# Optimization experiments

Hardware: AMD Instinct MI355X
Metric: run time of the kernel (lower is better)

Reference implementation:

```python
import jax, jax.numpy as jnp
import numpy as np

EPS = 1e-6

def _ln(x):
    # LayerNorm without affine, biased variance (matches torch default)
    m = jnp.mean(x, axis=-1, keepdims=True)
    v = jnp.var(x, axis=-1, keepdims=True)
    return (x - m) / jnp.sqrt(v + EPS)

def setup_inputs() -> dict:
    key = jax.random.key(0)
    ks = jax.random.split(key, 12)
    B, N, C = 8, 4096, 768
    H = C * 4
    s = 0.02
    return {
        "x":   jax.random.normal(ks[0], (B, N, C), dtype=jnp.float32),
        "Wq":  jax.random.normal(ks[1], (C, C), dtype=jnp.float32) * s,
        "bq":  jnp.zeros((C,), dtype=jnp.float32),
        "Wkv": jax.random.normal(ks[2], (C, 2 * C), dtype=jnp.float32) * s,
        "bkv": jnp.zeros((2 * C,), dtype=jnp.float32),
        "Wo":  jax.random.normal(ks[3], (C, C), dtype=jnp.float32) * s,
        "bo":  jnp.zeros((C,), dtype=jnp.float32),
        "W1":  jax.random.normal(ks[4], (C, H), dtype=jnp.float32) * s,
        "b1":  jnp.zeros((H,), dtype=jnp.float32),
        "W2":  jax.random.normal(ks[5], (H, C), dtype=jnp.float32) * s,
        "b2":  jnp.zeros((C,), dtype=jnp.float32),
    }

def reference(x, Wq, bq, Wkv, bkv, Wo, bo, W1, b1, W2, b2):
    B, N, C = x.shape
    h = 16
    d = C // h
    scale = d ** -0.5

    xn = _ln(x)                          # norm1 over full sequence
    past = xn[:, :-1, :]                 # [B, N-1, C]
    cur = xn[:, -1, :]                   # [B, C]

    q = (cur @ Wq + bq).reshape(B, h, 1, d)                 # [B,h,1,d]
    kv = past @ Wkv + bkv                                   # [B,N-1,2C]
    k, v = jnp.split(kv, 2, axis=-1)
    k = k.reshape(B, N - 1, h, d).transpose(0, 2, 1, 3)     # [B,h,N-1,d]
    v = v.reshape(B, N - 1, h, d).transpose(0, 2, 1, 3)

    sim = jnp.einsum('bhqd,bhkd->bhqk', q, k) * scale       # [B,h,1,N-1]
    attn = jax.nn.softmax(sim, axis=-1)
    out = jnp.einsum('bhqk,bhkd->bhqd', attn, v)            # [B,h,1,d]
    out = out.transpose(0, 2, 1, 3).reshape(B, C)           # [B,C]
    out = out @ Wo + bo

    last = x[:, -1, :] + out                                # attn residual
    mlp = jax.nn.gelu(_ln(last) @ W1 + b1, approximate=True) @ W2 + b2
    last = last + mlp                                       # mlp residual

    return x.at[:, -1, :].set(last)
```

## Files before the change

kernel.cpp:

```cpp
#include <hip/hip_runtime.h>

#define B_ 8
#define N_ 4096
#define C_ 768
#define NP_ 4095
#define H_ 16
#define D_ 48
#define HID_ 3072
#define SCALE 0.14433756729740643f

typedef unsigned short u16;
typedef unsigned int u32;
typedef __attribute__((ext_vector_type(4))) float f32x4;
typedef __attribute__((ext_vector_type(8))) short short8;

__device__ __forceinline__ u32 f2bf_bits(float f){
  union { float f; u32 i; } v; v.f = f;
  return (v.i + 0x7fffu + ((v.i >> 16) & 1u)) >> 16;
}
__device__ __forceinline__ u16 f2bf(float f){ return (u16)f2bf_bits(f); }
__device__ __forceinline__ float bf2f(u16 u){
  union { u32 i; float f; } v; v.i = ((u32)u) << 16; return v.f;
}
__device__ __forceinline__ u32 pack2(float a, float b){
  return f2bf_bits(a) | (f2bf_bits(b) << 16);
}

__global__ __launch_bounds__(256) void k_q(const float* __restrict__ x,
    const float* __restrict__ Wq, const float* __restrict__ bq,
    float* __restrict__ qv, float* __restrict__ zbase)
{
  int b = blockIdx.y, t = threadIdx.x;
  int j0 = blockIdx.x*32;
  {
    int gid = (b*24 + blockIdx.x)*256 + t;
    for (int u = gid; u < 98688; u += 49152) zbase[u] = 0.f;
  }
  __shared__ float xs[C_];
  __shared__ float red[32][9];
  __shared__ float redA[4], redB[4];
  const float* xr = x + ((size_t)b*N_ + NP_)*C_;
  float v0 = xr[t], v1 = xr[t+256], v2 = xr[t+512];
  float s = v0+v1+v2, q = v0*v0+v1*v1+v2*v2;
  #pragma unroll
  for (int off=32; off; off>>=1){ s += __shfl_xor(s,off); q += __shfl_xor(q,off); }
  int w = t>>6, l = t&63;
  if (l==0){ redA[w]=s; redB[w]=q; }
  __syncthreads();
  s = redA[0]+redA[1]+redA[2]+redA[3];
  q = redB[0]+redB[1]+redB[2]+redB[3];
  float mean = s*(1.f/C_), var = q*(1.f/C_) - mean*mean;
  float rstd = rsqrtf(var + 1e-6f);
  xs[t] = (v0-mean)*rstd; xs[t+256] = (v1-mean)*rstd; xs[t+512] = (v2-mean)*rstd;
  __syncthreads();
  int jl = t&31, part = t>>5;
  const float* wp = Wq + (size_t)(part*96)*C_ + j0 + jl;
  const float* xp = xs + part*96;
  float acc = 0.f;
  #pragma unroll 8
  for (int c=0;c<96;c++) acc += xp[c]*wp[(size_t)c*C_];
  red[jl][part] = acc;
  __syncthreads();
  if (part==0){
    float a = bq[j0+jl];
    #pragma unroll
    for (int p=0;p<8;p++) a += red[jl][p];
    qv[(size_t)b*C_ + j0 + jl] = a;
  }
}

__global__ __launch_bounds__(256) void k_qw(const float* __restrict__ qv,
    const float* __restrict__ Wkv, u16* __restrict__ qWb,
    float* __restrict__ qwsum)
{
  int b = blockIdx.y, t = threadIdx.x;
  int c0 = blockIdx.x*16;
  __shared__ float qs[C_];
  __shared__ float red2[16][17];
  for (int u=t; u<C_; u+=256) qs[u] = qv[(size_t)b*C_+u];
  __syncthreads();
  int h = t&15, cl = t>>4;
  int c = c0 + cl;
  const float* wp = Wkv + (size_t)c*(2*C_) + h*D_;
  const float* qh = qs + h*D_;
  float acc = 0.f;
  #pragma unroll
  for (int d=0; d<D_; d++) acc += qh[d]*wp[d];
  u16 wb = f2bf(acc);
  qWb[((size_t)b*H_ + h)*C_ + c] = wb;
  red2[h][cl] = bf2f(wb);
  __syncthreads();
  if (t < 16){
    float s2 = 0.f;
    #pragma unroll
    for (int j=0;j<16;j++) s2 += red2[t][j];
    atomicAdd(qwsum + (size_t)b*H_ + t, s2);
  }
}

__global__ __launch_bounds__(256) void k_sim(const float* __restrict__ x,
    const u16* __restrict__ qWb, const float* __restrict__ qwsum,
    u16* __restrict__ wrsT, float* __restrict__ denom, float* __restrict__ corr)
{
  int b = blockIdx.y;
  int tid = threadIdx.x;
  int w = tid>>6, l = tid&63;
  int kblk = (blockIdx.x*4 + w)*16;
  int r = l&15;
  int ko = (l>>4)*8;
  const float* ar = x + ((size_t)b*N_ + kblk + r)*C_ + ko;
  const u16*  br = qWb + ((size_t)b*H_ + r)*C_ + ko;
  f32x4 acc = {0.f,0.f,0.f,0.f};
  float s = 0.f, q = 0.f;
  #pragma unroll 8
  for (int s2=0;s2<24;s2++){
    float4 a0 = *(const float4*)(ar + s2*32);
    float4 a1 = *(const float4*)(ar + s2*32 + 4);
    union{uint4 u; short8 v;} A, Bf;
    A.u.x = pack2(a0.x, a0.y);
    A.u.y = pack2(a0.z, a0.w);
    A.u.z = pack2(a1.x, a1.y);
    A.u.w = pack2(a1.z, a1.w);
    Bf.u = *(const uint4*)(br + s2*32);
    acc = __builtin_amdgcn_mfma_f32_16x16x32_bf16(A.v, Bf.v, acc, 0,0,0);
    s += a0.x+a0.y+a0.z+a0.w + a1.x+a1.y+a1.z+a1.w;
    q += a0.x*a0.x+a0.y*a0.y+a0.z*a0.z+a0.w*a0.w
       + a1.x*a1.x+a1.y*a1.y+a1.z*a1.z+a1.w*a1.w;
  }
  s += __shfl_xor(s,16); q += __shfl_xor(q,16);
  s += __shfl_xor(s,32); q += __shfl_xor(q,32);
  float mean = s*(1.f/C_), var = q*(1.f/C_) - mean*mean;
  float rstd = rsqrtf(var + 1e-6f);
  int hh = l&15, mb = (l>>4)*4;
  float qs = qwsum[(size_t)b*H_ + hh];
  float dsum = 0.f, csum = 0.f;
  u16* wp = wrsT + ((size_t)b*H_ + hh)*N_ + kblk + mb;
  #pragma unroll
  for (int r4=0;r4<4;r4++){
    int m = mb + r4;
    int kt = kblk + m;
    float m_mean = __shfl(mean, m);
    float m_rstd = __shfl(rstd, m);
    float logit = m_rstd * (acc[r4] - m_mean*qs);
    float wv = (kt < NP_) ? __expf(logit*SCALE) : 0.f;
    u16 wb = f2bf(wv * m_rstd);
    wp[r4] = wb;
    dsum += wv;
    csum += bf2f(wb) * m_mean;
  }
  dsum += __shfl_xor(dsum,16); csum += __shfl_xor(csum,16);
  dsum += __shfl_xor(dsum,32); csum += __shfl_xor(csum,32);
  if (l < 16){
    atomicAdd(denom + (size_t)b*H_ + l, dsum);
    atomicAdd(corr  + (size_t)b*H_ + l, csum);
  }
}

__global__ __launch_bounds__(256) void k_ctx2(const float* __restrict__ x,
    const u16* __restrict__ wrsT, float* __restrict__ ctx)
{
  int b = blockIdx.y;
  int cg = blockIdx.x % 12;
  int ks = blockIdx.x / 12;
  int tid = threadIdx.x;
  int w = tid>>6, l = tid&63;
  int ctile = cg*64 + w*16;
  int k0 = ks*256;
  const size_t xb = (size_t)b*N_*C_;
  const u16* ap = wrsT + ((size_t)b*H_ + (l&15))*N_ + k0 + (l>>4)*8;
  const float* bp = x + xb + (size_t)(k0 + (l>>4)*8)*C_ + ctile + (l&15);
  f32x4 acc = {0.f,0.f,0.f,0.f};
  #pragma unroll 4
  for (int s=0;s<8;s++){
    union{uint4 u; short8 v;} A, Bf;
    A.u = *(const uint4*)(ap + s*32);
    const float* bq2 = bp + (size_t)s*32*C_;
    float x0 = bq2[0];
    float x1 = bq2[(size_t)1*C_];
    float x2 = bq2[(size_t)2*C_];
    float x3 = bq2[(size_t)3*C_];
    float x4 = bq2[(size_t)4*C_];
    float x5 = bq2[(size_t)5*C_];
    float x6 = bq2[(size_t)6*C_];
    float x7 = bq2[(size_t)7*C_];
    uint4 nb;
    nb.x = pack2(x0,x1); nb.y = pack2(x2,x3);
    nb.z = pack2(x4,x5); nb.w = pack2(x6,x7);
    Bf.u = nb;
    acc = __builtin_amdgcn_mfma_f32_16x16x32_bf16(A.v, Bf.v, acc, 0,0,0);
  }
  int cc = ctile + (l&15);
  float* cb = ctx + (size_t)b*H_*C_;
  #pragma unroll
  for (int r=0;r<4;r++){
    int h = (l>>4)*4 + r;
    atomicAdd(cb + h*C_ + cc, acc[r]);
  }
}

__global__ __launch_bounds__(256) void k_v(const float* __restrict__ ctx,
    const float* __restrict__ denom, const float* __restrict__ corr,
    const float* __restrict__ Wkv, const float* __restrict__ bkv,
    float* __restrict__ oat)
{
  int b = blockIdx.y, t = threadIdx.x;
  int t0 = blockIdx.x*32;
  int h0 = t0/D_;
  int h1 = (t0+31)/D_; if (h1 > H_-1) h1 = H_-1;
  __shared__ float cn[2][C_];
  __shared__ float red[32][9];
  float inv0 = 1.f/denom[(size_t)b*H_+h0];
  float inv1 = 1.f/denom[(size_t)b*H_+h1];
  float cr0 = corr[(size_t)b*H_+h0];
  float cr1 = corr[(size_t)b*H_+h1];
  for (int u=t; u<C_; u+=256){
    cn[0][u] = (ctx[((size_t)b*H_+h0)*C_+u] - cr0)*inv0;
    cn[1][u] = (ctx[((size_t)b*H_+h1)*C_+u] - cr1)*inv1;
  }
  __syncthreads();
  int jl = t&31, part = t>>5;
  int tt = t0 + jl;
  int hi = (tt/D_) - h0;
  const float* wp = Wkv + (size_t)(part*96)*(2*C_) + C_ + tt;
  const float* cp = cn[hi] + part*96;
  float acc = 0.f;
  #pragma unroll 8
  for (int c=0;c<96;c++) acc += cp[c]*wp[(size_t)c*(2*C_)];
  red[jl][part] = acc;
  __syncthreads();
  if (part==0){
    float a = bkv[C_ + tt];
    #pragma unroll
    for (int p=0;p<8;p++) a += red[jl][p];
    oat[(size_t)b*C_ + tt] = a;
  }
}

__global__ __launch_bounds__(256) void k_o(const float* __restrict__ x,
    const float* __restrict__ oat, const float* __restrict__ Wo,
    const float* __restrict__ bo, float* __restrict__ lastb)
{
  int b = blockIdx.y, t = threadIdx.x;
  int t0 = blockIdx.x*32;
  __shared__ float xs[C_];
  __shared__ float red[32][9];
  for (int u=t; u<C_; u+=256) xs[u] = oat[(size_t)b*C_+u];
  __syncthreads();
  int jl = t&31, part = t>>5;
  int tt = t0 + jl;
  const float* wp = Wo + (size_t)(part*96)*C_ + tt;
  const float* xp = xs + part*96;
  float acc = 0.f;
  #pragma unroll 8
  for (int c=0;c<96;c++) acc += xp[c]*wp[(size_t)c*C_];
  red[jl][part] = acc;
  __syncthreads();
  if (part==0){
    float a = bo[tt];
    #pragma unroll
    for (int p=0;p<8;p++) a += red[jl][p];
    lastb[(size_t)b*C_ + tt] = x[((size_t)b*N_ + NP_)*C_ + tt] + a;
  }
}

__global__ __launch_bounds__(256) void k_mlp1(const float* __restrict__ lastb,
    const float* __restrict__ W1, const float* __restrict__ b1,
    float* __restrict__ hid)
{
  int t = threadIdx.x;
  int j0 = blockIdx.x*16;
  __shared__ float xs[B_][C_];
  __shared__ float red[16][16][8];
  {
    int bb = t>>5, sub = t&31;
    const float* xr = lastb + (size_t)bb*C_;
    float s=0.f, q=0.f;
    #pragma unroll
    for (int j=0;j<24;j++){ float v = xr[sub+32*j]; s += v; q += v*v; }
    #pragma unroll
    for (int off=1; off<32; off<<=1){ s += __shfl_xor(s,off); q += __shfl_xor(q,off); }
    float mean = s*(1.f/C_), var = q*(1.f/C_) - mean*mean;
    float rstd = rsqrtf(var + 1e-6f);
    #pragma unroll
    for (int j=0;j<24;j++){ xs[bb][sub+32*j] = (xr[sub+32*j]-mean)*rstd; }
  }
  __syncthreads();
  int jl = t&15, part = t>>4;
  const float* wp = W1 + (size_t)(part*48)*HID_ + j0 + jl;
  float acc[B_];
  #pragma unroll
  for (int bb=0;bb<B_;bb++) acc[bb]=0.f;
  for (int c=0;c<48;c++){
    float wv = wp[(size_t)c*HID_];
    int cc = part*48 + c;
    #pragma unroll
    for (int bb=0;bb<B_;bb++) acc[bb] += xs[bb][cc]*wv;
  }
  #pragma unroll
  for (int bb=0;bb<B_;bb++) red[jl][part][bb] = acc[bb];
  __syncthreads();
  if (t < 128){
    int jl2 = t&15, bb = t>>4;
    float a = b1[j0+jl2];
    #pragma unroll
    for (int p=0;p<16;p++) a += red[jl2][p][bb];
    float t3 = a + 0.044715f*a*a*a;
    float g = 0.5f*a*(1.f + tanhf(0.7978845608f*t3));
    hid[(size_t)bb*HID_ + j0 + jl2] = g;
  }
}

__global__ __launch_bounds__(256) void k_mlp2(const float* __restrict__ hid,
    const float* __restrict__ W2, const float* __restrict__ b2,
    const float* __restrict__ lastb, float* __restrict__ outp)
{
  int t = threadIdx.x;
  int c0 = blockIdx.x*8;
  __shared__ float red[8][32][8];
  int ccl = t&7, part = t>>3;
  const float* wp = W2 + (size_t)(part*96)*C_ + c0 + ccl;
  float acc[B_];
  #pragma unroll
  for (int bb=0;bb<B_;bb++) acc[bb]=0.f;
  for (int j=0;j<96;j++){
    float wv = wp[(size_t)j*C_];
    int jj = part*96 + j;
    #pragma unroll
    for (int bb=0;bb<B_;bb++) acc[bb] += hid[(size_t)bb*HID_ + jj]*wv;
  }
  #pragma unroll
  for (int bb=0;bb<B_;bb++) red[ccl][part][bb] = acc[bb];
  __syncthreads();
  if (t < 64){
    int cc2 = t&7, bb = t>>3;
    float a = 0.f;
    #pragma unroll
    for (int p=0;p<32;p++) a += red[cc2][p][bb];
    int cc = c0 + cc2;
    a += b2[cc] + lastb[(size_t)bb*C_ + cc];
    outp[((size_t)bb*N_ + NP_)*C_ + cc] = a;
  }
}

extern "C" void kernel_launch(void* const* d_in, const int* in_sizes, int n_in,
                              void* d_out, int out_size, void* d_ws, size_t ws_size,
                              hipStream_t stream)
{
  (void)in_sizes; (void)n_in; (void)out_size; (void)ws_size;
  const float* x   = (const float*)d_in[0];
  const float* Wq  = (const float*)d_in[1];
  const float* bq  = (const float*)d_in[2];
  const float* Wkv = (const float*)d_in[3];
  const float* bkv = (const float*)d_in[4];
  const float* Wo  = (const float*)d_in[5];
  const float* bo  = (const float*)d_in[6];
  const float* W1  = (const float*)d_in[7];
  const float* b1  = (const float*)d_in[8];
  const float* W2  = (const float*)d_in[9];
  const float* b2  = (const float*)d_in[10];
  float* outp = (float*)d_out;
  float* ws = (float*)d_ws;
  float* ctx    = ws;
  float* denom  = ctx + 98304;
  float* corr   = denom + 128;
  float* qwsum  = corr + 128;
  float* qv     = qwsum + 128;
  float* oat    = qv + 6144;
  float* lastb  = oat + 6144;
  float* hid    = lastb + 6144;
  u16*   qWb    = (u16*)(hid + 24576);
  u16*   wrsT   = (u16*)(hid + 24576 + 49152);

  hipMemcpyAsync(outp, x, (size_t)B_*N_*C_*sizeof(float),
                 hipMemcpyDeviceToDevice, stream);
  hipLaunchKernelGGL(k_q,    dim3(24,B_), dim3(256), 0, stream, x, Wq, bq, qv, ctx);
  hipLaunchKernelGGL(k_qw,   dim3(48,B_), dim3(256), 0, stream, qv, Wkv, qWb, qwsum);
  hipLaunchKernelGGL(k_sim,  dim3(64,B_), dim3(256), 0, stream, x, qWb, qwsum, wrsT, denom, corr);
  hipLaunchKernelGGL(k_ctx2, dim3(192,B_), dim3(256), 0, stream, x, wrsT, ctx);
  hipLaunchKernelGGL(k_v,    dim3(24,B_), dim3(256), 0, stream, ctx, denom, corr, Wkv, bkv, oat);
  hipLaunchKernelGGL(k_o,    dim3(24,B_), dim3(256), 0, stream, x, oat, Wo, bo, lastb);
  hipLaunchKernelGGL(k_mlp1, dim3(192), dim3(256), 0, stream, lastb, W1, b1, hid);
  hipLaunchKernelGGL(k_mlp2, dim3(96), dim3(256), 0, stream, hid, W2, b2, lastb, outp);
}
```

Baseline: 130.4 us.

## Fuse output copy into k_sim and batch q projections across all batches

Drops the separate device-to-device memcpy of x into the output. k_sim now writes each x tile it already loads straight to the output buffer, which saves one full read of the large activation tensor. k_q and k_qw now process all 8 batches in one block grid, so each Wq and Wkv element is read once instead of once per batch. The cost is more shared memory and registers in the small kernels, fewer blocks for those kernels, and extra write traffic inside k_sim.

```diff
diff --git a/kernel.cpp b/kernel.cpp
--- a/kernel.cpp
+++ b/kernel.cpp
@@ -30,42 +30,49 @@
     const float* __restrict__ Wq, const float* __restrict__ bq,
     float* __restrict__ qv, float* __restrict__ zbase)
 {
-  int b = blockIdx.y, t = threadIdx.x;
+  int t = threadIdx.x;
   int j0 = blockIdx.x*32;
   {
-    int gid = (b*24 + blockIdx.x)*256 + t;
-    for (int u = gid; u < 98688; u += 49152) zbase[u] = 0.f;
-  }
-  __shared__ float xs[C_];
-  __shared__ float red[32][9];
-  __shared__ float redA[4], redB[4];
-  const float* xr = x + ((size_t)b*N_ + NP_)*C_;
-  float v0 = xr[t], v1 = xr[t+256], v2 = xr[t+512];
-  float s = v0+v1+v2, q = v0*v0+v1*v1+v2*v2;
-  #pragma unroll
-  for (int off=32; off; off>>=1){ s += __shfl_xor(s,off); q += __shfl_xor(q,off); }
-  int w = t>>6, l = t&63;
-  if (l==0){ redA[w]=s; redB[w]=q; }
-  __syncthreads();
-  s = redA[0]+redA[1]+redA[2]+redA[3];
-  q = redB[0]+redB[1]+redB[2]+redB[3];
-  float mean = s*(1.f/C_), var = q*(1.f/C_) - mean*mean;
-  float rstd = rsqrtf(var + 1e-6f);
-  xs[t] = (v0-mean)*rstd; xs[t+256] = (v1-mean)*rstd; xs[t+512] = (v2-mean)*rstd;
+    int gid = blockIdx.x*256 + t;
+    for (int u = gid; u < 98688; u += 6144) zbase[u] = 0.f;
+  }
+  __shared__ float xs[B_][C_];
+  __shared__ float red[32][9][8];
+  {
+    int bb = t>>5, sub = t&31;
+    const float* xr = x + ((size_t)bb*N_ + NP_)*C_;
+    float v[24];
+    float s=0.f, q=0.f;
+    #pragma unroll
+    for (int j=0;j<24;j++){ v[j] = xr[sub+32*j]; s += v[j]; q += v[j]*v[j]; }
+    #pragma unroll
+    for (int off=1; off<32; off<<=1){ s += __shfl_xor(s,off); q += __shfl_xor(q,off); }
+    float mean = s*(1.f/C_), var = q*(1.f/C_) - mean*mean;
+    float rstd = rsqrtf(var + 1e-6f);
+    #pragma unroll
+    for (int j=0;j<24;j++) xs[bb][sub+32*j] = (v[j]-mean)*rstd;
+  }
   __syncthreads();
   int jl = t&31, part = t>>5;
   const float* wp = Wq + (size_t)(part*96)*C_ + j0 + jl;
-  const float* xp = xs + part*96;
-  float acc = 0.f;
-  #pragma unroll 8
-  for (int c=0;c<96;c++) acc += xp[c]*wp[(size_t)c*C_];
-  red[jl][part] = acc;
-  __syncthreads();
-  if (part==0){
-    float a = bq[j0+jl];
-    #pragma unroll
-    for (int p=0;p<8;p++) a += red[jl][p];
-    qv[(size_t)b*C_ + j0 + jl] = a;
+  float acc[B_];
+  #pragma unroll
+  for (int bb=0;bb<B_;bb++) acc[bb]=0.f;
+  for (int c=0;c<96;c++){
+    float wv = wp[(size_t)c*C_];
+    int cc = part*96 + c;
+    #pragma unroll
+    for (int bb=0;bb<B_;bb++) acc[bb] += xs[bb][cc]*wv;
+  }
+  #pragma unroll
+  for (int bb=0;bb<B_;bb++) red[jl][part][bb] = acc[bb];
+  __syncthreads();
+  {
+    int jl2 = t&31, bb = t>>5;
+    float a = bq[j0+jl2];
+    #pragma unroll
+    for (int p=0;p<8;p++) a += red[jl2][p][bb];
+    qv[(size_t)bb*C_ + j0 + jl2] = a;
   }
 }
 
@@ -73,34 +80,44 @@
     const float* __restrict__ Wkv, u16* __restrict__ qWb,
     float* __restrict__ qwsum)
 {
-  int b = blockIdx.y, t = threadIdx.x;
+  int t = threadIdx.x;
   int c0 = blockIdx.x*16;
-  __shared__ float qs[C_];
-  __shared__ float red2[16][17];
-  for (int u=t; u<C_; u+=256) qs[u] = qv[(size_t)b*C_+u];
+  __shared__ float qs[B_*C_];
+  __shared__ float red2[B_][16][17];
+  for (int u=t; u<B_*C_; u+=256) qs[u] = qv[u];
   __syncthreads();
   int h = t&15, cl = t>>4;
   int c = c0 + cl;
   const float* wp = Wkv + (size_t)c*(2*C_) + h*D_;
-  const float* qh = qs + h*D_;
-  float acc = 0.f;
-  #pragma unroll
-  for (int d=0; d<D_; d++) acc += qh[d]*wp[d];
-  u16 wb = f2bf(acc);
-  qWb[((size_t)b*H_ + h)*C_ + c] = wb;
-  red2[h][cl] = bf2f(wb);
-  __syncthreads();
-  if (t < 16){
+  float acc[B_];
+  #pragma unroll
+  for (int bb=0;bb<B_;bb++) acc[bb]=0.f;
+  #pragma unroll 8
+  for (int d=0; d<D_; d++){
+    float wv = wp[d];
+    #pragma unroll
+    for (int bb=0;bb<B_;bb++) acc[bb] += qs[bb*C_ + h*D_ + d]*wv;
+  }
+  #pragma unroll
+  for (int bb=0;bb<B_;bb++){
+    u16 wb = f2bf(acc[bb]);
+    qWb[((size_t)bb*H_ + h)*C_ + c] = wb;
+    red2[bb][h][cl] = bf2f(wb);
+  }
+  __syncthreads();
+  if (t < 128){
+    int bb = t>>4, hh = t&15;
     float s2 = 0.f;
     #pragma unroll
-    for (int j=0;j<16;j++) s2 += red2[t][j];
-    atomicAdd(qwsum + (size_t)b*H_ + t, s2);
+    for (int j=0;j<16;j++) s2 += red2[bb][hh][j];
+    atomicAdd(qwsum + (size_t)bb*H_ + hh, s2);
   }
 }
 
 __global__ __launch_bounds__(256) void k_sim(const float* __restrict__ x,
     const u16* __restrict__ qWb, const float* __restrict__ qwsum,
-    u16* __restrict__ wrsT, float* __restrict__ denom, float* __restrict__ corr)
+    float* __restrict__ outp, u16* __restrict__ wrsT,
+    float* __restrict__ denom, float* __restrict__ corr)
 {
   int b = blockIdx.y;
   int tid = threadIdx.x;
@@ -108,7 +125,9 @@
   int kblk = (blockIdx.x*4 + w)*16;
   int r = l&15;
   int ko = (l>>4)*8;
-  const float* ar = x + ((size_t)b*N_ + kblk + r)*C_ + ko;
+  const size_t roff = ((size_t)b*N_ + kblk + r)*C_ + ko;
+  const float* ar = x + roff;
+  float* op = outp + roff;
   const u16*  br = qWb + ((size_t)b*H_ + r)*C_ + ko;
   f32x4 acc = {0.f,0.f,0.f,0.f};
   float s = 0.f, q = 0.f;
@@ -116,6 +135,8 @@
   for (int s2=0;s2<24;s2++){
     float4 a0 = *(const float4*)(ar + s2*32);
     float4 a1 = *(const float4*)(ar + s2*32 + 4);
+    *(float4*)(op + s2*32)     = a0;
+    *(float4*)(op + s2*32 + 4) = a1;
     union{uint4 u; short8 v;} A, Bf;
     A.u.x = pack2(a0.x, a0.y);
     A.u.y = pack2(a0.z, a0.w);
@@ -371,11 +392,9 @@
   u16*   qWb    = (u16*)(hid + 24576);
   u16*   wrsT   = (u16*)(hid + 24576 + 49152);
 
-  hipMemcpyAsync(outp, x, (size_t)B_*N_*C_*sizeof(float),
-                 hipMemcpyDeviceToDevice, stream);
-  hipLaunchKernelGGL(k_q,    dim3(24,B_), dim3(256), 0, stream, x, Wq, bq, qv, ctx);
-  hipLaunchKernelGGL(k_qw,   dim3(48,B_), dim3(256), 0, stream, qv, Wkv, qWb, qwsum);
-  hipLaunchKernelGGL(k_sim,  dim3(64,B_), dim3(256), 0, stream, x, qWb, qwsum, wrsT, denom, corr);
+  hipLaunchKernelGGL(k_q,    dim3(24), dim3(256), 0, stream, x, Wq, bq, qv, ctx);
+  hipLaunchKernelGGL(k_qw,   dim3(48), dim3(256), 0, stream, qv, Wkv, qWb, qwsum);
+  hipLaunchKernelGGL(k_sim,  dim3(64,B_), dim3(256), 0, stream, x, qWb, qwsum, outp, wrsT, denom, corr);
   hipLaunchKernelGGL(k_ctx2, dim3(192,B_), dim3(256), 0, stream, x, wrsT, ctx);
   hipLaunchKernelGGL(k_v,    dim3(24,B_), dim3(256), 0, stream, ctx, denom, corr, Wkv, bkv, oat);
   hipLaunchKernelGGL(k_o,    dim3(24,B_), dim3(256), 0, stream, x, oat, Wo, bo, lastb);
```

New measurement: 114.0 us. 12.6% less time.
